# Optimization experiments

Measured on AMD Instinct MI355X. Metric: run time of the kernel, lower is better.

The kernel has to match this reference:

```python
import jax, jax.numpy as jnp
import numpy as np

N = 50000   # nodes
E = 800000  # edges (before self-loops)
D = 256     # hidden_dim
H = 8       # heads
C = D // H  # 32 channels per head
NEG_SLOPE = 0.2


def setup_inputs() -> dict:
    key = jax.random.key(0)
    ks = jax.random.split(key, 10)
    sc = 0.05
    x = jax.random.normal(ks[0], (N, D), dtype=jnp.float32)
    edges_idx = jax.random.randint(ks[1], (2, E), 0, N, dtype=jnp.int64)
    # GATv2Conv params per layer: lin_l (W for source j), lin_r (W for target i), att [H,C], bias [H*C]
    Wl1 = jax.random.normal(ks[2], (D, H * C), dtype=jnp.float32) * sc
    Wr1 = jax.random.normal(ks[3], (D, H * C), dtype=jnp.float32) * sc
    att1 = jax.random.normal(ks[4], (H, C), dtype=jnp.float32) * sc
    b1 = jnp.zeros((H * C,), dtype=jnp.float32)
    Wl2 = jax.random.normal(ks[5], (D, H * C), dtype=jnp.float32) * sc
    Wr2 = jax.random.normal(ks[6], (D, H * C), dtype=jnp.float32) * sc
    att2 = jax.random.normal(ks[7], (H, C), dtype=jnp.float32) * sc
    b2 = jnp.zeros((H * C,), dtype=jnp.float32)
    return dict(x=x, edges_idx=edges_idx, Wl1=Wl1, Wr1=Wr1, att1=att1, b1=b1,
                Wl2=Wl2, Wr2=Wr2, att2=att2, b2=b2)


def gatv2_layer(x, src, dst, Wl, Wr, att, b):
    # x: [N, D]; src/dst: [E'] (self-loops included)
    xl = (x @ Wl).reshape(-1, H, C)  # source-side transform
    xr = (x @ Wr).reshape(-1, H, C)  # target-side transform
    # GATv2 score: e_ij = a^T LeakyReLU(Wl x_j + Wr x_i)
    z = jax.nn.leaky_relu(xl[src] + xr[dst], NEG_SLOPE)   # [E', H, C]
    e = jnp.einsum('ehc,hc->eh', z, att)                  # [E', H]
    # softmax over edges sharing the same target node (segment softmax)
    m = jax.ops.segment_max(e, dst, num_segments=N)       # [N, H]
    ex = jnp.exp(e - m[dst])
    s = jax.ops.segment_sum(ex, dst, num_segments=N)      # [N, H]
    alpha = ex / s[dst]                                   # [E', H]
    out = jax.ops.segment_sum(alpha[..., None] * xl[src], dst, num_segments=N)  # [N, H, C]
    return out.reshape(-1, H * C) + b


def reference(x, edges_idx, Wl1, Wr1, att1, b1, Wl2, Wr2, att2, b2):
    # PyG default add_self_loops=True
    loop = jnp.arange(N, dtype=edges_idx.dtype)
    src = jnp.concatenate([edges_idx[0], loop])
    dst = jnp.concatenate([edges_idx[1], loop])
    # layer 1 -> ELU -> layer 2 (dropout identity in eval mode)
    h = jax.nn.elu(gatv2_layer(x, src, dst, Wl1, Wr1, att1, b1))
    return gatv2_layer(h, src, dst, Wl2, Wr2, att2, b2)
```

## Files before the change

kernel.cpp:

```cpp
#include <hip/hip_runtime.h>
#include <hip/hip_bf16.h>
#include <math.h>

#define HEADS 8
#define HC 256
#define NEG_SLOPE 0.2f

typedef __attribute__((ext_vector_type(8))) short short8;
typedef __attribute__((ext_vector_type(16))) float floatx16;

__device__ inline ushort bf16_rne(float f) {
    unsigned u = __float_as_uint(f);
    return (ushort)((u + 0x7FFFu + ((u >> 16) & 1u)) >> 16);
}

__global__ __launch_bounds__(256) void cvt_bf16_sw(
        const float* __restrict__ x, ushort* __restrict__ xb, long long nblk) {
    long long id = (long long)blockIdx.x * blockDim.x + threadIdx.x;
    if (id >= nblk) return;
    long long r = id >> 5;
    int j = (int)(id & 31);
    const float4* p = (const float4*)(x + id * 8);
    float4 a = p[0], b = p[1];
    short8 pk;
    pk[0] = (short)bf16_rne(a.x); pk[1] = (short)bf16_rne(a.y);
    pk[2] = (short)bf16_rne(a.z); pk[3] = (short)bf16_rne(a.w);
    pk[4] = (short)bf16_rne(b.x); pk[5] = (short)bf16_rne(b.y);
    pk[6] = (short)bf16_rne(b.z); pk[7] = (short)bf16_rne(b.w);
    int jx = j ^ ((int)r & 7);
    *(short8*)(xb + r * 256 + jx * 8) = pk;
}

__global__ __launch_bounds__(256) void build_wt(
        const float* __restrict__ Wl, const float* __restrict__ Wr,
        ushort* __restrict__ wt) {
    int n = blockIdx.x;
    int k = threadIdx.x;
    const float* W = (n < 256) ? Wl : Wr;
    int col = n & 255;
    int jx = (k >> 3) ^ (n & 7);
    wt[n * HC + jx * 8 + (k & 7)] = bf16_rne(W[k * HC + col]);
}

__global__ __launch_bounds__(256) void gemm_mfma(
        const ushort* __restrict__ A, const ushort* __restrict__ wt,
        ushort* __restrict__ xl, ushort* __restrict__ xr, int N) {
    __shared__ ushort lA[64 * 256];
    __shared__ ushort lB[64 * 256];
    int local = blockIdx.x & 127;
    int grp   = blockIdx.x >> 7;
    int mt = grp * 16 + (local & 15);
    int nt = local >> 4;
    int m0 = mt * 64, n0 = nt * 64;
    int t = threadIdx.x;
    int lane = t & 63, wv = t >> 6;

    {
        const ushort* gA = A + (long long)m0 * HC;
        const ushort* gB = wt + (long long)n0 * HC;
        #pragma unroll
        for (int i = 0; i < 8; ++i) {
            int off = (wv * 8 + i) * 512;
            __builtin_amdgcn_global_load_lds(
                (const __attribute__((address_space(1))) unsigned int*)(gA + off + lane * 8),
                (__attribute__((address_space(3))) unsigned int*)(lA + off), 16, 0, 0);
            __builtin_amdgcn_global_load_lds(
                (const __attribute__((address_space(1))) unsigned int*)(gB + off + lane * 8),
                (__attribute__((address_space(3))) unsigned int*)(lB + off), 16, 0, 0);
        }
    }
    __syncthreads();

    int rA = (wv & 1) * 32 + (lane & 31);
    int rB = (wv >> 1) * 32 + (lane & 31);
    int kh = lane >> 5;
    int sA = rA & 7, sB = rB & 7;
    floatx16 acc;
    #pragma unroll
    for (int i = 0; i < 16; ++i) acc[i] = 0.f;
    #pragma unroll
    for (int step = 0; step < 16; ++step) {
        int j = step * 2 + kh;
        short8 a = *(const short8*)&lA[rA * 256 + ((j ^ sA) * 8)];
        short8 b = *(const short8*)&lB[rB * 256 + ((j ^ sB) * 8)];
        acc = __builtin_amdgcn_mfma_f32_32x32x16_bf16(a, b, acc, 0, 0, 0);
    }

    ushort* obase = (nt < 4) ? xl : xr;
    int colb = (n0 & 255) + (wv >> 1) * 32 + (lane & 31);
    int rbase = m0 + (wv & 1) * 32 + 4 * kh;
    #pragma unroll
    for (int g = 0; g < 4; ++g) {
        #pragma unroll
        for (int q = 0; q < 4; ++q) {
            int row = rbase + q + 8 * g;
            if (row < N)
                obase[(long long)row * HC + colb] = bf16_rne(acc[g * 4 + q]);
        }
    }
}

__global__ void hist_dst(const int* __restrict__ eidx, int E, int N,
                         int* __restrict__ counts) {
    int w = blockIdx.x * blockDim.x + threadIdx.x;
    int Etot = E + N;
    if (w >= Etot) return;
    int d = (w < E) ? eidx[E + w] : (w - E);
    atomicAdd(&counts[d], 1);
}

__global__ __launch_bounds__(1024) void scan_local(
        const int* __restrict__ counts, int* __restrict__ rowptr,
        int* __restrict__ bsum, int N) {
    __shared__ int wsums[16];
    int t = threadIdx.x, lane = t & 63, wv = t >> 6;
    int i = blockIdx.x * 1024 + t;
    int v = (i < N) ? counts[i] : 0;
    int orig = v;
    #pragma unroll
    for (int off = 1; off < 64; off <<= 1) {
        int n = __shfl_up(v, off, 64);
        if (lane >= off) v += n;
    }
    if (lane == 63) wsums[wv] = v;
    __syncthreads();
    int woff = 0, total = 0;
    #pragma unroll
    for (int w_ = 0; w_ < 16; ++w_) {
        int s = wsums[w_];
        if (w_ < wv) woff += s;
        total += s;
    }
    if (i < N) rowptr[i] = v + woff - orig;
    if (t == 0) bsum[blockIdx.x] = total;
}

__global__ void scan_bsums(const int* __restrict__ bsum, int* __restrict__ bsum2,
                           int* __restrict__ rowptr, int nb, int N) {
    int lane = threadIdx.x;
    int v = (lane < nb) ? bsum[lane] : 0;
    int orig = v;
    #pragma unroll
    for (int off = 1; off < 64; off <<= 1) {
        int n = __shfl_up(v, off, 64);
        if (lane >= off) v += n;
    }
    if (lane < nb) bsum2[lane] = v - orig;
    if (lane == 63) rowptr[N] = v;
}

__global__ __launch_bounds__(1024) void scan_add(
        int* __restrict__ rowptr, const int* __restrict__ bsum2, int N) {
    int i = blockIdx.x * 1024 + threadIdx.x;
    if (i < N) rowptr[i] += bsum2[blockIdx.x];
}

__global__ void scatter_edges(const int* __restrict__ eidx, int E, int N,
                              const int* __restrict__ rowptr,
                              int* __restrict__ fill, int* __restrict__ srcS) {
    int w = blockIdx.x * blockDim.x + threadIdx.x;
    int Etot = E + N;
    if (w >= Etot) return;
    int s, d;
    if (w < E) { s = eidx[w]; d = eidx[E + w]; }
    else       { s = w - E;   d = w - E; }
    int pos = rowptr[d] + atomicAdd(&fill[d], 1);
    srcS[pos] = s << 9;
}

template <int LAYER1>
__global__ __launch_bounds__(256) void gat_node(
        const ushort* __restrict__ xl, const ushort* __restrict__ xr,
        const float* __restrict__ att, const float* __restrict__ bias,
        const int* __restrict__ rowptr, const unsigned* __restrict__ srcB,
        void* __restrict__ outp, int N) {
    int lane = threadIdx.x & 63;
    int h = lane >> 5;
    int q = lane & 31;
    unsigned cb = (unsigned)q * 16u;
    const char* xbase = (const char*)xl;

    float4 av0 = *(const float4*)(att + q * 8);
    float4 av1 = *(const float4*)(att + q * 8 + 4);
    float4 bv0 = *(const float4*)(bias + q * 8);
    float4 bv1 = *(const float4*)(bias + q * 8 + 4);

    int nodeStride = gridDim.x * 4;
    for (int node = blockIdx.x * 4 + (threadIdx.x >> 6); node < N;
         node += nodeStride) {
        int beg = rowptr[node], end = rowptr[node + 1];

        long long nbase = (long long)node * HC;
        uint4 xu = *(const uint4*)(xr + nbase + q * 8);
        float xr0 = __uint_as_float(xu.x << 16);
        float xr1 = __uint_as_float(xu.x & 0xffff0000u);
        float xr2 = __uint_as_float(xu.y << 16);
        float xr3 = __uint_as_float(xu.y & 0xffff0000u);
        float xr4 = __uint_as_float(xu.z << 16);
        float xr5 = __uint_as_float(xu.z & 0xffff0000u);
        float xr6 = __uint_as_float(xu.w << 16);
        float xr7 = __uint_as_float(xu.w & 0xffff0000u);

        float ssA = 0.f, ssB = 0.f;
        float aA0 = 0.f, aA1 = 0.f, aA2 = 0.f, aA3 = 0.f;
        float aA4 = 0.f, aA5 = 0.f, aA6 = 0.f, aA7 = 0.f;
        float aB0 = 0.f, aB1 = 0.f, aB2 = 0.f, aB3 = 0.f;
        float aB4 = 0.f, aB5 = 0.f, aB6 = 0.f, aB7 = 0.f;

#define EDGE2(P, SFX, ALLV)                                                    \
    {                                                                          \
        int pe = (P) + ((ALLV) ? h : 0);                                       \
        unsigned off = srcB[pe] | cb;                                          \
        uint4 dv = *(const uint4*)(xbase + off);                               \
        float v0 = __uint_as_float(dv.x << 16);                                \
        float v1 = __uint_as_float(dv.x & 0xffff0000u);                        \
        float v2 = __uint_as_float(dv.y << 16);                                \
        float v3 = __uint_as_float(dv.y & 0xffff0000u);                        \
        float v4 = __uint_as_float(dv.z << 16);                                \
        float v5 = __uint_as_float(dv.z & 0xffff0000u);                        \
        float v6 = __uint_as_float(dv.w << 16);                                \
        float v7 = __uint_as_float(dv.w & 0xffff0000u);                        \
        float t0 = v0 + xr0, t1 = v1 + xr1, t2 = v2 + xr2, t3 = v3 + xr3;      \
        float t4 = v4 + xr4, t5 = v5 + xr5, t6 = v6 + xr6, t7 = v7 + xr7;      \
        float st = av0.x * t0;                                                 \
        st = fmaf(av0.y, t1, st); st = fmaf(av0.z, t2, st);                    \
        st = fmaf(av0.w, t3, st); st = fmaf(av1.x, t4, st);                    \
        st = fmaf(av1.y, t5, st); st = fmaf(av1.z, t6, st);                    \
        st = fmaf(av1.w, t7, st);                                              \
        float sa = av0.x * fabsf(t0);                                          \
        sa = fmaf(av0.y, fabsf(t1), sa); sa = fmaf(av0.z, fabsf(t2), sa);      \
        sa = fmaf(av0.w, fabsf(t3), sa); sa = fmaf(av1.x, fabsf(t4), sa);      \
        sa = fmaf(av1.y, fabsf(t5), sa); sa = fmaf(av1.z, fabsf(t6), sa);      \
        sa = fmaf(av1.w, fabsf(t7), sa);                                       \
        float sc = fmaf(0.6f, st, 0.4f * sa);                                  \
        sc += __shfl_xor(sc, 1, 64);                                           \
        sc += __shfl_xor(sc, 2, 64);                                           \
        float ex = ((ALLV) || h == 0) ? __expf(sc) : 0.f;                      \
        ss##SFX += ex;                                                         \
        a##SFX##0 = fmaf(ex, v0, a##SFX##0);                                   \
        a##SFX##1 = fmaf(ex, v1, a##SFX##1);                                   \
        a##SFX##2 = fmaf(ex, v2, a##SFX##2);                                   \
        a##SFX##3 = fmaf(ex, v3, a##SFX##3);                                   \
        a##SFX##4 = fmaf(ex, v4, a##SFX##4);                                   \
        a##SFX##5 = fmaf(ex, v5, a##SFX##5);                                   \
        a##SFX##6 = fmaf(ex, v6, a##SFX##6);                                   \
        a##SFX##7 = fmaf(ex, v7, a##SFX##7);                                   \
    }

        int p = beg;
        for (; p + 4 <= end; p += 4) {
            EDGE2(p, A, 1)
            EDGE2(p + 2, B, 1)
        }
        if (p + 2 <= end) { EDGE2(p, A, 1) p += 2; }
        if (p < end) { EDGE2(p, B, 0) }
#undef EDGE2

        float ss = ssA + ssB;
        ss += __shfl_xor(ss, 32, 64);
        float a0 = aA0 + aB0; a0 += __shfl_xor(a0, 32, 64);
        float a1 = aA1 + aB1; a1 += __shfl_xor(a1, 32, 64);
        float a2 = aA2 + aB2; a2 += __shfl_xor(a2, 32, 64);
        float a3 = aA3 + aB3; a3 += __shfl_xor(a3, 32, 64);
        float a4 = aA4 + aB4; a4 += __shfl_xor(a4, 32, 64);
        float a5 = aA5 + aB5; a5 += __shfl_xor(a5, 32, 64);
        float a6 = aA6 + aB6; a6 += __shfl_xor(a6, 32, 64);
        float a7 = aA7 + aB7; a7 += __shfl_xor(a7, 32, 64);

        float inv = 1.f / ss;
        float o0 = fmaf(a0, inv, bv0.x);
        float o1 = fmaf(a1, inv, bv0.y);
        float o2 = fmaf(a2, inv, bv0.z);
        float o3 = fmaf(a3, inv, bv0.w);
        float o4 = fmaf(a4, inv, bv1.x);
        float o5 = fmaf(a5, inv, bv1.y);
        float o6 = fmaf(a6, inv, bv1.z);
        float o7 = fmaf(a7, inv, bv1.w);

        if (LAYER1) {
            float s0 = h ? o4 : o0;
            float s1 = h ? o5 : o1;
            float s2 = h ? o6 : o2;
            float s3 = h ? o7 : o3;
            s0 = s0 > 0.f ? s0 : expm1f(s0);
            s1 = s1 > 0.f ? s1 : expm1f(s1);
            s2 = s2 > 0.f ? s2 : expm1f(s2);
            s3 = s3 > 0.f ? s3 : expm1f(s3);
            ushort4 pk;
            pk.x = bf16_rne(s0); pk.y = bf16_rne(s1);
            pk.z = bf16_rne(s2); pk.w = bf16_rne(s3);
            int jx = q ^ (node & 7);
            *(ushort4*)((ushort*)outp + nbase + jx * 8 + h * 4) = pk;
        } else {
            float4 ov = h ? make_float4(o4, o5, o6, o7)
                          : make_float4(o0, o1, o2, o3);
            *(float4*)((float*)outp + nbase + q * 8 + h * 4) = ov;
        }
    }
}

extern "C" void kernel_launch(void* const* d_in, const int* in_sizes, int n_in,
                              void* d_out, int out_size, void* d_ws, size_t ws_size,
                              hipStream_t stream) {
    const float* x    = (const float*)d_in[0];
    const int*   eidx = (const int*)d_in[1];
    const float* Wl1  = (const float*)d_in[2];
    const float* Wr1  = (const float*)d_in[3];
    const float* att1 = (const float*)d_in[4];
    const float* b1   = (const float*)d_in[5];
    const float* Wl2  = (const float*)d_in[6];
    const float* Wr2  = (const float*)d_in[7];
    const float* att2 = (const float*)d_in[8];
    const float* b2   = (const float*)d_in[9];
    float* out = (float*)d_out;

    const int N = in_sizes[0] / HC;
    const int E = in_sizes[1] / 2;
    const int Etot = E + N;
    const long long NHC = (long long)N * HC;

    ushort* xl   = (ushort*)d_ws;
    ushort* xr   = xl + NHC;
    ushort* hbuf = xr + NHC;
    ushort* xb   = hbuf + NHC;
    ushort* wt1  = xb + NHC;
    ushort* wt2  = wt1 + 512 * HC;
    int* rowptr  = (int*)(wt2 + 512 * HC);
    int* counts  = rowptr + (N + 1);
    int* fill    = counts + N;
    int* bsum    = fill + N;
    int* bsum2   = bsum + 64;
    int* srcS    = bsum2 + 64;

    const int TB = 256;
    dim3 blk(TB);
    int gEdgesT = (Etot + TB - 1) / TB;
    int mtTiles = (N + 63) / 64;
    int gGemm   = ((mtTiles + 15) / 16) * 128;
    int gNode   = 3136;
    int nb      = (N + 1023) / 1024;
    long long nblk = NHC / 8;
    int gCvt    = (int)((nblk + TB - 1) / TB);

    cvt_bf16_sw<<<gCvt, blk, 0, stream>>>(x, xb, nblk);
    build_wt<<<512, blk, 0, stream>>>(Wl1, Wr1, wt1);
    build_wt<<<512, blk, 0, stream>>>(Wl2, Wr2, wt2);
    hipMemsetAsync(counts, 0, (size_t)2 * N * sizeof(int), stream);
    hist_dst<<<gEdgesT, blk, 0, stream>>>(eidx, E, N, counts);
    scan_local<<<nb, 1024, 0, stream>>>(counts, rowptr, bsum, N);
    scan_bsums<<<1, 64, 0, stream>>>(bsum, bsum2, rowptr, nb, N);
    scan_add<<<nb, 1024, 0, stream>>>(rowptr, bsum2, N);
    scatter_edges<<<gEdgesT, blk, 0, stream>>>(eidx, E, N, rowptr, fill, srcS);

    gemm_mfma<<<gGemm, blk, 0, stream>>>(xb, wt1, xl, xr, N);
    gat_node<1><<<gNode, blk, 0, stream>>>(xl, xr, att1, b1, rowptr,
                                           (const unsigned*)srcS, hbuf, N);

    gemm_mfma<<<gGemm, blk, 0, stream>>>(hbuf, wt2, xl, xr, N);
    gat_node<0><<<gNode, blk, 0, stream>>>(xl, xr, att2, b2, rowptr,
                                           (const unsigned*)srcS, out, N);
}
```

Baseline: 431.0 us.

## Use 128x128 double-buffered GEMM tiles and one-node-per-wave GAT grid

The GEMM switches from 64x64 tiles that load the full K=256 into LDS at once to 128x128 tiles. These stream K in four 64-wide chunks through double-buffered LDS, and each wave computes a 2x2 block of 32x32 MFMA accumulators. This raises operand reuse per LDS load and overlaps global loads with MFMA work, at the cost of more registers and more synchronisation. The GAT node kernel drops its grid-stride loop and launches one wave per node, removing loop overhead and the fixed grid size.

Measured after the change: 407.7 us. -5.4%, faster.

```diff
diff --git a/kernel.cpp b/kernel.cpp
--- a/kernel.cpp
+++ b/kernel.cpp
@@ -45,57 +45,90 @@
 __global__ __launch_bounds__(256) void gemm_mfma(
         const ushort* __restrict__ A, const ushort* __restrict__ wt,
         ushort* __restrict__ xl, ushort* __restrict__ xr, int N) {
-    __shared__ ushort lA[64 * 256];
-    __shared__ ushort lB[64 * 256];
-    int local = blockIdx.x & 127;
-    int grp   = blockIdx.x >> 7;
-    int mt = grp * 16 + (local & 15);
-    int nt = local >> 4;
-    int m0 = mt * 64, n0 = nt * 64;
+    __shared__ ushort lA[2][128 * 64];
+    __shared__ ushort lB[2][128 * 64];
+    int mtT = (N + 127) >> 7;
+    int local = blockIdx.x & 31;
+    int grp   = blockIdx.x >> 5;
+    int mt = grp * 8 + (local & 7);
+    int nt = local >> 3;
+    if (mt >= mtT) return;
+    int m0 = mt * 128, n0 = nt * 128;
     int t = threadIdx.x;
     int lane = t & 63, wv = t >> 6;
 
-    {
-        const ushort* gA = A + (long long)m0 * HC;
-        const ushort* gB = wt + (long long)n0 * HC;
+    int gOff = (lane >> 3) * 512 + (lane & 7) * 16;
+    const char* gA = (const char*)A + (long long)m0 * 512;
+    const char* gB = (const char*)wt + (long long)n0 * 512;
+
+#define STAGE(BUF, KS)                                                         \
+    {                                                                          \
+        _Pragma("unroll")                                                      \
+        for (int i_ = 0; i_ < 4; ++i_) {                                       \
+            int rr = wv * 32 + i_ * 8;                                         \
+            __builtin_amdgcn_global_load_lds(                                  \
+                (const __attribute__((address_space(1))) unsigned int*)        \
+                    (gA + (long long)rr * 512 + (KS) * 128 + gOff),            \
+                (__attribute__((address_space(3))) unsigned int*)              \
+                    (&lA[BUF][rr * 64]), 16, 0, 0);                            \
+            __builtin_amdgcn_global_load_lds(                                  \
+                (const __attribute__((address_space(1))) unsigned int*)        \
+                    (gB + (long long)rr * 512 + (KS) * 128 + gOff),            \
+                (__attribute__((address_space(3))) unsigned int*)              \
+                    (&lB[BUF][rr * 64]), 16, 0, 0);                            \
+        }                                                                      \
+    }
+
+    int rA0 = (wv & 1) * 64 + (lane & 31);
+    int rB0 = (wv >> 1) * 64 + (lane & 31);
+    int kh = lane >> 5;
+    int sA = rA0 & 7, sB = rB0 & 7;
+    floatx16 ac00, ac01, ac10, ac11;
+    #pragma unroll
+    for (int i = 0; i < 16; ++i) { ac00[i] = 0.f; ac01[i] = 0.f;
+                                   ac10[i] = 0.f; ac11[i] = 0.f; }
+
+    STAGE(0, 0)
+    __syncthreads();
+    int buf = 0;
+    #pragma unroll
+    for (int ks = 0; ks < 4; ++ks) {
+        if (ks < 3) STAGE(buf ^ 1, ks + 1)
         #pragma unroll
-        for (int i = 0; i < 8; ++i) {
-            int off = (wv * 8 + i) * 512;
-            __builtin_amdgcn_global_load_lds(
-                (const __attribute__((address_space(1))) unsigned int*)(gA + off + lane * 8),
-                (__attribute__((address_space(3))) unsigned int*)(lA + off), 16, 0, 0);
-            __builtin_amdgcn_global_load_lds(
-                (const __attribute__((address_space(1))) unsigned int*)(gB + off + lane * 8),
-                (__attribute__((address_space(3))) unsigned int*)(lB + off), 16, 0, 0);
+        for (int kk = 0; kk < 4; ++kk) {
+            int jb = kk * 2 + kh;
+            short8 a0 = *(const short8*)&lA[buf][rA0 * 64 + ((jb ^ sA) * 8)];
+            short8 a1 = *(const short8*)&lA[buf][(rA0 + 32) * 64 + ((jb ^ sA) * 8)];
+            short8 b0 = *(const short8*)&lB[buf][rB0 * 64 + ((jb ^ sB) * 8)];
+            short8 b1 = *(const short8*)&lB[buf][(rB0 + 32) * 64 + ((jb ^ sB) * 8)];
+            ac00 = __builtin_amdgcn_mfma_f32_32x32x16_bf16(a0, b0, ac00, 0, 0, 0);
+            ac01 = __builtin_amdgcn_mfma_f32_32x32x16_bf16(a0, b1, ac01, 0, 0, 0);
+            ac10 = __builtin_amdgcn_mfma_f32_32x32x16_bf16(a1, b0, ac10, 0, 0, 0);
+            ac11 = __builtin_amdgcn_mfma_f32_32x32x16_bf16(a1, b1, ac11, 0, 0, 0);
         }
-    }
-    __syncthreads();
-
-    int rA = (wv & 1) * 32 + (lane & 31);
-    int rB = (wv >> 1) * 32 + (lane & 31);
-    int kh = lane >> 5;
-    int sA = rA & 7, sB = rB & 7;
-    floatx16 acc;
-    #pragma unroll
-    for (int i = 0; i < 16; ++i) acc[i] = 0.f;
-    #pragma unroll
-    for (int step = 0; step < 16; ++step) {
-        int j = step * 2 + kh;
-        short8 a = *(const short8*)&lA[rA * 256 + ((j ^ sA) * 8)];
-        short8 b = *(const short8*)&lB[rB * 256 + ((j ^ sB) * 8)];
-        acc = __builtin_amdgcn_mfma_f32_32x32x16_bf16(a, b, acc, 0, 0, 0);
-    }
-
-    ushort* obase = (nt < 4) ? xl : xr;
-    int colb = (n0 & 255) + (wv >> 1) * 32 + (lane & 31);
-    int rbase = m0 + (wv & 1) * 32 + 4 * kh;
+        __syncthreads();
+        buf ^= 1;
+    }
+#undef STAGE
+
+    ushort* obase = (nt < 2) ? xl : xr;
+    int colb = (nt & 1) * 128 + (wv >> 1) * 64 + (lane & 31);
+    int rbase = m0 + (wv & 1) * 64 + 4 * kh;
     #pragma unroll
     for (int g = 0; g < 4; ++g) {
         #pragma unroll
         for (int q = 0; q < 4; ++q) {
-            int row = rbase + q + 8 * g;
-            if (row < N)
-                obase[(long long)row * HC + colb] = bf16_rne(acc[g * 4 + q]);
+            int row0 = rbase + q + 8 * g;
+            int row1 = row0 + 32;
+            int e = g * 4 + q;
+            if (row0 < N) {
+                obase[(long long)row0 * HC + colb]      = bf16_rne(ac00[e]);
+                obase[(long long)row0 * HC + colb + 32] = bf16_rne(ac01[e]);
+            }
+            if (row1 < N) {
+                obase[(long long)row1 * HC + colb]      = bf16_rne(ac10[e]);
+                obase[(long long)row1 * HC + colb + 32] = bf16_rne(ac11[e]);
+            }
         }
     }
 }
@@ -174,38 +207,33 @@
         const float* __restrict__ att, const float* __restrict__ bias,
         const int* __restrict__ rowptr, const unsigned* __restrict__ srcB,
         void* __restrict__ outp, int N) {
+    int node = blockIdx.x * 4 + (threadIdx.x >> 6);
     int lane = threadIdx.x & 63;
+    if (node >= N) return;
     int h = lane >> 5;
     int q = lane & 31;
     unsigned cb = (unsigned)q * 16u;
     const char* xbase = (const char*)xl;
-
+    int beg = rowptr[node], end = rowptr[node + 1];
+
+    long long nbase = (long long)node * HC;
+    uint4 xu = *(const uint4*)(xr + nbase + q * 8);
+    float xr0 = __uint_as_float(xu.x << 16);
+    float xr1 = __uint_as_float(xu.x & 0xffff0000u);
+    float xr2 = __uint_as_float(xu.y << 16);
+    float xr3 = __uint_as_float(xu.y & 0xffff0000u);
+    float xr4 = __uint_as_float(xu.z << 16);
+    float xr5 = __uint_as_float(xu.z & 0xffff0000u);
+    float xr6 = __uint_as_float(xu.w << 16);
+    float xr7 = __uint_as_float(xu.w & 0xffff0000u);
     float4 av0 = *(const float4*)(att + q * 8);
     float4 av1 = *(const float4*)(att + q * 8 + 4);
-    float4 bv0 = *(const float4*)(bias + q * 8);
-    float4 bv1 = *(const float4*)(bias + q * 8 + 4);
-
-    int nodeStride = gridDim.x * 4;
-    for (int node = blockIdx.x * 4 + (threadIdx.x >> 6); node < N;
-         node += nodeStride) {
-        int beg = rowptr[node], end = rowptr[node + 1];
-
-        long long nbase = (long long)node * HC;
-        uint4 xu = *(const uint4*)(xr + nbase + q * 8);
-        float xr0 = __uint_as_float(xu.x << 16);
-        float xr1 = __uint_as_float(xu.x & 0xffff0000u);
-        float xr2 = __uint_as_float(xu.y << 16);
-        float xr3 = __uint_as_float(xu.y & 0xffff0000u);
-        float xr4 = __uint_as_float(xu.z << 16);
-        float xr5 = __uint_as_float(xu.z & 0xffff0000u);
-        float xr6 = __uint_as_float(xu.w << 16);
-        float xr7 = __uint_as_float(xu.w & 0xffff0000u);
-
-        float ssA = 0.f, ssB = 0.f;
-        float aA0 = 0.f, aA1 = 0.f, aA2 = 0.f, aA3 = 0.f;
-        float aA4 = 0.f, aA5 = 0.f, aA6 = 0.f, aA7 = 0.f;
-        float aB0 = 0.f, aB1 = 0.f, aB2 = 0.f, aB3 = 0.f;
-        float aB4 = 0.f, aB5 = 0.f, aB6 = 0.f, aB7 = 0.f;
+
+    float ssA = 0.f, ssB = 0.f;
+    float aA0 = 0.f, aA1 = 0.f, aA2 = 0.f, aA3 = 0.f;
+    float aA4 = 0.f, aA5 = 0.f, aA6 = 0.f, aA7 = 0.f;
+    float aB0 = 0.f, aB1 = 0.f, aB2 = 0.f, aB3 = 0.f;
+    float aB4 = 0.f, aB5 = 0.f, aB6 = 0.f, aB7 = 0.f;
 
 #define EDGE2(P, SFX, ALLV)                                                    \
     {                                                                          \
@@ -247,55 +275,56 @@
         a##SFX##7 = fmaf(ex, v7, a##SFX##7);                                   \
     }
 
-        int p = beg;
-        for (; p + 4 <= end; p += 4) {
-            EDGE2(p, A, 1)
-            EDGE2(p + 2, B, 1)
-        }
-        if (p + 2 <= end) { EDGE2(p, A, 1) p += 2; }
-        if (p < end) { EDGE2(p, B, 0) }
+    int p = beg;
+    for (; p + 4 <= end; p += 4) {
+        EDGE2(p, A, 1)
+        EDGE2(p + 2, B, 1)
+    }
+    if (p + 2 <= end) { EDGE2(p, A, 1) p += 2; }
+    if (p < end) { EDGE2(p, B, 0) }
 #undef EDGE2
 
-        float ss = ssA + ssB;
-        ss += __shfl_xor(ss, 32, 64);
-        float a0 = aA0 + aB0; a0 += __shfl_xor(a0, 32, 64);
-        float a1 = aA1 + aB1; a1 += __shfl_xor(a1, 32, 64);
-        float a2 = aA2 + aB2; a2 += __shfl_xor(a2, 32, 64);
-        float a3 = aA3 + aB3; a3 += __shfl_xor(a3, 32, 64);
-        float a4 = aA4 + aB4; a4 += __shfl_xor(a4, 32, 64);
-        float a5 = aA5 + aB5; a5 += __shfl_xor(a5, 32, 64);
-        float a6 = aA6 + aB6; a6 += __shfl_xor(a6, 32, 64);
-        float a7 = aA7 + aB7; a7 += __shfl_xor(a7, 32, 64);
-
-        float inv = 1.f / ss;
-        float o0 = fmaf(a0, inv, bv0.x);
-        float o1 = fmaf(a1, inv, bv0.y);
-        float o2 = fmaf(a2, inv, bv0.z);
-        float o3 = fmaf(a3, inv, bv0.w);
-        float o4 = fmaf(a4, inv, bv1.x);
-        float o5 = fmaf(a5, inv, bv1.y);
-        float o6 = fmaf(a6, inv, bv1.z);
-        float o7 = fmaf(a7, inv, bv1.w);
-
-        if (LAYER1) {
-            float s0 = h ? o4 : o0;
-            float s1 = h ? o5 : o1;
-            float s2 = h ? o6 : o2;
-            float s3 = h ? o7 : o3;
-            s0 = s0 > 0.f ? s0 : expm1f(s0);
-            s1 = s1 > 0.f ? s1 : expm1f(s1);
-            s2 = s2 > 0.f ? s2 : expm1f(s2);
-            s3 = s3 > 0.f ? s3 : expm1f(s3);
-            ushort4 pk;
-            pk.x = bf16_rne(s0); pk.y = bf16_rne(s1);
-            pk.z = bf16_rne(s2); pk.w = bf16_rne(s3);
-            int jx = q ^ (node & 7);
-            *(ushort4*)((ushort*)outp + nbase + jx * 8 + h * 4) = pk;
-        } else {
-            float4 ov = h ? make_float4(o4, o5, o6, o7)
-                          : make_float4(o0, o1, o2, o3);
-            *(float4*)((float*)outp + nbase + q * 8 + h * 4) = ov;
-        }
+    float ss = ssA + ssB;
+    ss += __shfl_xor(ss, 32, 64);
+    float a0 = aA0 + aB0; a0 += __shfl_xor(a0, 32, 64);
+    float a1 = aA1 + aB1; a1 += __shfl_xor(a1, 32, 64);
+    float a2 = aA2 + aB2; a2 += __shfl_xor(a2, 32, 64);
+    float a3 = aA3 + aB3; a3 += __shfl_xor(a3, 32, 64);
+    float a4 = aA4 + aB4; a4 += __shfl_xor(a4, 32, 64);
+    float a5 = aA5 + aB5; a5 += __shfl_xor(a5, 32, 64);
+    float a6 = aA6 + aB6; a6 += __shfl_xor(a6, 32, 64);
+    float a7 = aA7 + aB7; a7 += __shfl_xor(a7, 32, 64);
+
+    float inv = 1.f / ss;
+    float4 bv0 = *(const float4*)(bias + q * 8);
+    float4 bv1 = *(const float4*)(bias + q * 8 + 4);
+    float o0 = fmaf(a0, inv, bv0.x);
+    float o1 = fmaf(a1, inv, bv0.y);
+    float o2 = fmaf(a2, inv, bv0.z);
+    float o3 = fmaf(a3, inv, bv0.w);
+    float o4 = fmaf(a4, inv, bv1.x);
+    float o5 = fmaf(a5, inv, bv1.y);
+    float o6 = fmaf(a6, inv, bv1.z);
+    float o7 = fmaf(a7, inv, bv1.w);
+
+    if (LAYER1) {
+        float s0 = h ? o4 : o0;
+        float s1 = h ? o5 : o1;
+        float s2 = h ? o6 : o2;
+        float s3 = h ? o7 : o3;
+        s0 = s0 > 0.f ? s0 : expm1f(s0);
+        s1 = s1 > 0.f ? s1 : expm1f(s1);
+        s2 = s2 > 0.f ? s2 : expm1f(s2);
+        s3 = s3 > 0.f ? s3 : expm1f(s3);
+        ushort4 pk;
+        pk.x = bf16_rne(s0); pk.y = bf16_rne(s1);
+        pk.z = bf16_rne(s2); pk.w = bf16_rne(s3);
+        int jx = q ^ (node & 7);
+        *(ushort4*)((ushort*)outp + nbase + jx * 8 + h * 4) = pk;
+    } else {
+        float4 ov = h ? make_float4(o4, o5, o6, o7)
+                      : make_float4(o0, o1, o2, o3);
+        *(float4*)((float*)outp + nbase + q * 8 + h * 4) = ov;
     }
 }
 
@@ -335,9 +364,9 @@
     const int TB = 256;
     dim3 blk(TB);
     int gEdgesT = (Etot + TB - 1) / TB;
-    int mtTiles = (N + 63) / 64;
-    int gGemm   = ((mtTiles + 15) / 16) * 128;
-    int gNode   = 3136;
+    int mtTiles = (N + 127) / 128;
+    int gGemm   = ((mtTiles + 7) / 8) * 32;
+    int gNode   = (N + 3) / 4;
     int nb      = (N + 1023) / 1024;
     long long nblk = NHC / 8;
     int gCvt    = (int)((nblk + TB - 1) / TB);
```
